# Kernel optimization log

Measured on AMD Instinct MI355X. Metric: run time of the kernel, lower is better.

Reference implementation:

```python
import jax, jax.numpy as jnp
import numpy as np

N = 50000
E = 800000
IN_C, HID_C, OUT_C = 5, 64, 32


def setup_inputs() -> dict:
    key = jax.random.key(0)
    ks = jax.random.split(key, 9)
    x = jax.random.normal(ks[0], (N, IN_C), dtype=jnp.float32)
    edge_index = jax.random.randint(ks[1], (2, E), 0, N, dtype=jnp.int64)
    # SAGEConv params: lin_l (neighbor path, has bias), lin_r (root path, no bias)
    def lin(k, fan_out, fan_in):
        s = 1.0 / np.sqrt(fan_in)
        return jax.random.uniform(k, (fan_out, fan_in), jnp.float32, -s, s)
    W1l = lin(ks[2], HID_C, IN_C); b1 = jnp.zeros((HID_C,), jnp.float32); W1r = lin(ks[3], HID_C, IN_C)
    W2l = lin(ks[4], HID_C, HID_C); b2 = jnp.zeros((HID_C,), jnp.float32); W2r = lin(ks[5], HID_C, HID_C)
    W3l = lin(ks[6], OUT_C, HID_C); b3 = jnp.zeros((OUT_C,), jnp.float32); W3r = lin(ks[7], OUT_C, HID_C)
    return {"x": x, "edge_index": edge_index,
            "W1l": W1l, "b1": b1, "W1r": W1r,
            "W2l": W2l, "b2": b2, "W2r": W2r,
            "W3l": W3l, "b3": b3, "W3r": W3r}


def _sage_conv(x, src, dst, inv_deg, Wl, bl, Wr):
    # PyG SAGEConv (aggr='mean'): out = lin_l(mean_j x_j) + lin_r(x)
    msg = x[src]                                          # [E, d_in] gather
    agg = jax.ops.segment_sum(msg, dst, num_segments=N)   # [N, d_in] scatter-add
    mean = agg * inv_deg                                  # mean aggregation
    return mean @ Wl.T + bl + x @ Wr.T


def reference(x, edge_index, W1l, b1, W1r, W2l, b2, W2r, W3l, b3, W3r):
    src, dst = edge_index[0], edge_index[1]
    deg = jax.ops.segment_sum(jnp.ones((E,), x.dtype), dst, num_segments=N)
    inv_deg = (1.0 / jnp.maximum(deg, 1.0))[:, None]      # [N, 1]
    h = jax.nn.relu(_sage_conv(x, src, dst, inv_deg, W1l, b1, W1r))
    # F.dropout(p=0.2, training=self.training): identity in eval mode
    h = jax.nn.relu(_sage_conv(h, src, dst, inv_deg, W2l, b2, W2r))
    out = _sage_conv(h, src, dst, inv_deg, W3l, b3, W3r)
    return out
```

## Files before the change

### kernel.cpp

```cpp
#include <hip/hip_runtime.h>
#include <hip/hip_fp16.h>


#define N_NODES 50000
#define N_EDGES 800000
#define IN_C 5
#define HID_C 64
#define OUT_C 32

#define NB 196
#define BCAP 6144
#define BWG 256
#define BCH (N_EDGES / BWG)

typedef __attribute__((ext_vector_type(8))) short bf16x8;
typedef __attribute__((ext_vector_type(4))) float f32x4;

__device__ __forceinline__ int rfl(int v) { return __builtin_amdgcn_readfirstlane(v); }
__device__ __forceinline__ float lanebc(float v, int l) {
    return __int_as_float(__builtin_amdgcn_readlane(__float_as_int(v), l));
}
__device__ __forceinline__ unsigned short f2bf(float f) {
    unsigned u = __float_as_uint(f);
    return (unsigned short)((u + 0x7fffu + ((u >> 16) & 1u)) >> 16);
}
__device__ __forceinline__ float bf2f(unsigned short b) {
    return __uint_as_float(((unsigned)b) << 16);
}
__device__ __forceinline__ float2 unpk_h2(unsigned u) {
    __half2 h = *(__half2*)&u;
    return __half22float2(h);
}


__global__ __launch_bounds__(256) void k_bucket(const int* __restrict__ ei,
                                                int* __restrict__ gcur,
                                                unsigned* __restrict__ ebuf) {
    __shared__ int hist[NB];
    __shared__ int loff[NB];
    __shared__ int cur[NB];
    __shared__ int gbase[NB];
    __shared__ int scanb[256];
    __shared__ unsigned stage[BCH];
    const int t = threadIdx.x;
    const int c0 = blockIdx.x * BCH;

    if (t < NB) hist[t] = 0;
    __syncthreads();
    for (int i = t; i < BCH; i += 256) {
        int d = ei[N_EDGES + c0 + i];
        atomicAdd(&hist[d >> 8], 1);
    }
    __syncthreads();
    scanb[t] = (t < NB) ? hist[t] : 0;
    __syncthreads();
#pragma unroll
    for (int o = 1; o < 256; o <<= 1) {
        int v = scanb[t];
        int a = (t >= o) ? scanb[t - o] : 0;
        __syncthreads();
        scanb[t] = v + a;
        __syncthreads();
    }
    if (t < NB) {
        int ex = (t == 0) ? 0 : scanb[t - 1];
        loff[t] = ex;
        cur[t] = ex;
        gbase[t] = atomicAdd(&gcur[t], hist[t]);
    }
    __syncthreads();
    for (int i = t; i < BCH; i += 256) {
        int d = ei[N_EDGES + c0 + i];
        int s = ei[c0 + i];
        int b = d >> 8;
        int p = atomicAdd(&cur[b], 1);
        stage[p] = ((unsigned)d << 16) | (unsigned)s;
    }
    __syncthreads();
    for (int i = t; i < BCH; i += 256) {
        unsigned ev = stage[i];
        int b = ev >> 24;
        int pos = gbase[b] + (i - loff[b]);
        if (pos < BCAP) ebuf[b * BCAP + pos] = ev;
    }
}

__global__ __launch_bounds__(256) void k_bsort(const int* __restrict__ gcur,
                                               const unsigned* __restrict__ ebuf,
                                               int* __restrict__ row_off,
                                               float* __restrict__ inv_deg,
                                               int* __restrict__ srcs) {
    __shared__ int sc[256];
    __shared__ int cnt[256];
    __shared__ int loff[256];
    __shared__ int cur[256];
    __shared__ int stage[BCAP];
    const int t = threadIdx.x;
    const int b = blockIdx.x;

    sc[t] = (t < NB) ? gcur[t] : 0;
    __syncthreads();
#pragma unroll
    for (int o = 1; o < 256; o <<= 1) {
        int v = sc[t];
        int a = (t >= o) ? sc[t - o] : 0;
        __syncthreads();
        sc[t] = v + a;
        __syncthreads();
    }
    const int base = (b == 0) ? 0 : sc[b - 1];
    const int nraw = gcur[b];
    const int n = nraw < BCAP ? nraw : BCAP;
    const int node0 = b << 8;
    const unsigned* eb = ebuf + b * BCAP;

    cnt[t] = 0;
    __syncthreads();
    for (int i = t; i < n; i += 256) atomicAdd(&cnt[(eb[i] >> 16) & 255], 1);
    __syncthreads();
    loff[t] = cnt[t];
    __syncthreads();
#pragma unroll
    for (int o = 1; o < 256; o <<= 1) {
        int v = loff[t];
        int a = (t >= o) ? loff[t - o] : 0;
        __syncthreads();
        loff[t] = v + a;
        __syncthreads();
    }
    int ex = loff[t] - cnt[t];
    cur[t] = ex;
    int node = node0 + t;
    if (node < N_NODES) {
        row_off[node] = base + ex;
        int d = cnt[t];
        inv_deg[node] = 1.0f / (float)(d > 1 ? d : 1);
    }
    if (b == 0 && t == 0) row_off[N_NODES] = N_EDGES;
    __syncthreads();
    for (int i = t; i < n; i += 256) {
        unsigned ev = eb[i];
        int p = atomicAdd(&cur[(ev >> 16) & 255], 1);
        stage[p] = (int)(ev & 0xFFFFu);
    }
    __syncthreads();
    for (int i = t; i < n; i += 256) srcs[base + i] = stage[i];
}


__global__ __launch_bounds__(256) void k_prep(
    const float* __restrict__ W2l, const float* __restrict__ W2r,
    const float* __restrict__ W3l, const float* __restrict__ W3r,
    unsigned short* __restrict__ W2hi, unsigned short* __restrict__ W2lo,
    unsigned short* __restrict__ W3hi, unsigned short* __restrict__ W3lo,
    int* __restrict__ gcur) {
    int t = blockIdx.x * 256 + threadIdx.x;
    int stride = gridDim.x * 256;
    if (blockIdx.x == 0 && threadIdx.x < NB) gcur[threadIdx.x] = 0;
    for (int p = t; p < 64 * 128; p += stride) {
        int j = p >> 7, k = p & 127;
        float w = (k < 64) ? W2l[j * 64 + k] : W2r[j * 64 + (k - 64)];
        unsigned short h = f2bf(w);
        W2hi[p] = h;
        W2lo[p] = f2bf(w - bf2f(h));
    }
    for (int p = t; p < 32 * 128; p += stride) {
        int j = p >> 7, k = p & 127;
        float w = (k < 64) ? W3l[j * 64 + k] : W3r[j * 64 + (k - 64)];
        unsigned short h = f2bf(w);
        W3hi[p] = h;
        W3lo[p] = f2bf(w - bf2f(h));
    }
}


__global__ __launch_bounds__(512) void k_layer1(
    const float* __restrict__ x, const int* __restrict__ row_off,
    const int* __restrict__ srcs, const float* __restrict__ inv_deg,
    const float* __restrict__ W1l, const float* __restrict__ b1,
    const float* __restrict__ W1r, __half* __restrict__ h1) {
    const int t = threadIdx.x;
    const int lane = t & 63;
    const int v = blockIdx.x * 8 + (t >> 6);
    if (v >= N_NODES) return;
    const int sub = lane >> 3;
    const int c = lane & 7;

    float wl[IN_C], wr[IN_C];
#pragma unroll
    for (int i = 0; i < IN_C; ++i) {
        wl[i] = W1l[lane * IN_C + i];
        wr[i] = W1r[lane * IN_C + i];
    }
    float bb = b1[lane];

    int beg = rfl(row_off[v]);
    int end = rfl(row_off[v + 1]);
    float sum = 0.f;
    for (int e = beg; e < end; e += 8) {
        int o = e + sub;
        if (o < end && c < IN_C) sum += x[srcs[o] * IN_C + c];
    }
    sum += __shfl_xor(sum, 8, 64);
    sum += __shfl_xor(sum, 16, 64);
    sum += __shfl_xor(sum, 32, 64);
    float summ = sum * inv_deg[v];
    float xv = (lane < IN_C) ? x[v * IN_C + lane] : 0.f;
    float acc = bb;
#pragma unroll
    for (int i = 0; i < IN_C; ++i) {
        acc += wl[i] * lanebc(summ, i);
        acc += wr[i] * lanebc(xv, i);
    }
    h1[v * HID_C + lane] = __float2half(fmaxf(acc, 0.f));
}


template <typename T> __device__ __forceinline__ T cvt_out(float v);
template <> __device__ __forceinline__ float cvt_out<float>(float v) { return v; }
template <> __device__ __forceinline__ __half cvt_out<__half>(float v) { return __float2half(v); }

template <int DOUT, bool RELU, typename OutT>
__global__ __launch_bounds__(256) void k_fused(
    const __half* __restrict__ h, const int* __restrict__ row_off,
    const int* __restrict__ srcs, const float* __restrict__ inv_deg,
    const unsigned short* __restrict__ Whi, const unsigned short* __restrict__ Wlo,
    const float* __restrict__ bias, OutT* __restrict__ out) {
    constexpr int AP = 136;
    __shared__ __align__(16) unsigned short Ah[16][AP];
    __shared__ __align__(16) unsigned short Al[16][AP];
    const int t = threadIdx.x;
    const int lane = t & 63;
    const int w = t >> 6;
    const int ns = lane >> 4;
    const int cg = lane & 15;
    const int node0 = blockIdx.x * 16;
    const unsigned* h32 = (const unsigned*)h;

    const int m = w * 4 + ns;
    const int v = node0 + m;
    const int beg = row_off[v];
    const int deg = row_off[v + 1] - beg;
    const unsigned* rowb = h32 + cg * 2;

    float f0 = 0.f, f1 = 0.f, f2 = 0.f, f3 = 0.f;
    for (int k = 0; k < deg; k += 4) {
        int i0 = srcs[beg + k];
        int i1 = (k + 1 < deg) ? srcs[beg + k + 1] : i0;
        int i2 = (k + 2 < deg) ? srcs[beg + k + 2] : i0;
        int i3 = (k + 3 < deg) ? srcs[beg + k + 3] : i0;
        uint2 u0 = *(const uint2*)(rowb + i0 * 32);
        uint2 u1 = *(const uint2*)(rowb + i1 * 32);
        uint2 u2 = *(const uint2*)(rowb + i2 * 32);
        uint2 u3 = *(const uint2*)(rowb + i3 * 32);
        float2 a0 = unpk_h2(u0.x), b0 = unpk_h2(u0.y);
        f0 += a0.x; f1 += a0.y; f2 += b0.x; f3 += b0.y;
        if (k + 1 < deg) {
            float2 a = unpk_h2(u1.x), b = unpk_h2(u1.y);
            f0 += a.x; f1 += a.y; f2 += b.x; f3 += b.y;
        }
        if (k + 2 < deg) {
            float2 a = unpk_h2(u2.x), b = unpk_h2(u2.y);
            f0 += a.x; f1 += a.y; f2 += b.x; f3 += b.y;
        }
        if (k + 3 < deg) {
            float2 a = unpk_h2(u3.x), b = unpk_h2(u3.y);
            f0 += a.x; f1 += a.y; f2 += b.x; f3 += b.y;
        }
    }

    uint2 ur = *(const uint2*)(rowb + v * 32);
    float2 r0 = unpk_h2(ur.x), r1 = unpk_h2(ur.y);
    float idg = inv_deg[v];
    float m0 = f0 * idg, m1 = f1 * idg, m2 = f2 * idg, m3 = f3 * idg;

    {
        unsigned short a0 = f2bf(m0), a1 = f2bf(m1), a2 = f2bf(m2), a3 = f2bf(m3);
        uint2 hi, lo;
        hi.x = (unsigned)a0 | ((unsigned)a1 << 16);
        hi.y = (unsigned)a2 | ((unsigned)a3 << 16);
        lo.x = (unsigned)f2bf(m0 - bf2f(a0)) | ((unsigned)f2bf(m1 - bf2f(a1)) << 16);
        lo.y = (unsigned)f2bf(m2 - bf2f(a2)) | ((unsigned)f2bf(m3 - bf2f(a3)) << 16);
        *(uint2*)&Ah[m][cg * 4] = hi;
        *(uint2*)&Al[m][cg * 4] = lo;
    }
    {
        unsigned short a0 = f2bf(r0.x), a1 = f2bf(r0.y), a2 = f2bf(r1.x), a3 = f2bf(r1.y);
        uint2 hi, lo;
        hi.x = (unsigned)a0 | ((unsigned)a1 << 16);
        hi.y = (unsigned)a2 | ((unsigned)a3 << 16);
        lo.x = (unsigned)f2bf(r0.x - bf2f(a0)) | ((unsigned)f2bf(r0.y - bf2f(a1)) << 16);
        lo.y = (unsigned)f2bf(r1.x - bf2f(a2)) | ((unsigned)f2bf(r1.y - bf2f(a3)) << 16);
        *(uint2*)&Ah[m][64 + cg * 4] = hi;
        *(uint2*)&Al[m][64 + cg * 4] = lo;
    }
    __syncthreads();

    constexpr int NT = DOUT / 16;
    if (w < NT) {
        const int r = lane & 15;
        const int quad = lane >> 4;
        f32x4 acc = (f32x4){0.f, 0.f, 0.f, 0.f};
#pragma unroll
        for (int ks = 0; ks < 4; ++ks) {
            bf16x8 ah = *(const bf16x8*)&Ah[r][ks * 32 + quad * 8];
            bf16x8 al = *(const bf16x8*)&Al[r][ks * 32 + quad * 8];
            const size_t wb = ((size_t)(w * 16 + r)) * 128 + ks * 32 + quad * 8;
            bf16x8 bh = *(const bf16x8*)(Whi + wb);
            bf16x8 bl = *(const bf16x8*)(Wlo + wb);
            acc = __builtin_amdgcn_mfma_f32_16x16x32_bf16(ah, bh, acc, 0, 0, 0);
            acc = __builtin_amdgcn_mfma_f32_16x16x32_bf16(ah, bl, acc, 0, 0, 0);
            acc = __builtin_amdgcn_mfma_f32_16x16x32_bf16(al, bh, acc, 0, 0, 0);
        }
        float bv = bias[w * 16 + r];
#pragma unroll
        for (int g = 0; g < 4; ++g) {
            int mm = quad * 4 + g;
            float vv = acc[g] + bv;
            if (RELU) vv = fmaxf(vv, 0.f);
            out[(size_t)(node0 + mm) * DOUT + w * 16 + r] = cvt_out<OutT>(vv);
        }
    }
}


extern "C" void kernel_launch(void* const* d_in, const int* in_sizes, int n_in,
                              void* d_out, int out_size, void* d_ws, size_t ws_size,
                              hipStream_t stream) {
    const float* x   = (const float*)d_in[0];
    const int*   ei  = (const int*)d_in[1];
    const float* W1l = (const float*)d_in[2];
    const float* b1  = (const float*)d_in[3];
    const float* W1r = (const float*)d_in[4];
    const float* W2l = (const float*)d_in[5];
    const float* b2  = (const float*)d_in[6];
    const float* W2r = (const float*)d_in[7];
    const float* W3l = (const float*)d_in[8];
    const float* b3  = (const float*)d_in[9];
    const float* W3r = (const float*)d_in[10];

    char* ws = (char*)d_ws;
    size_t off = 0;
    auto alloc = [&](size_t bytes) -> char* {
        char* p = ws + off;
        off += (bytes + 255) & ~(size_t)255;
        return p;
    };
    int*      gcur   = (int*)alloc(NB * sizeof(int));
    int*      rowoff = (int*)alloc((N_NODES + 1) * sizeof(int));
    float*    invdeg = (float*)alloc(N_NODES * sizeof(float));
    int*      srcs   = (int*)alloc(N_EDGES * sizeof(int));
    unsigned* ebuf   = (unsigned*)alloc((size_t)NB * BCAP * sizeof(unsigned));
    __half*   h1     = (__half*)alloc((size_t)N_NODES * HID_C * sizeof(__half));
    __half*   h2     = (__half*)alloc((size_t)N_NODES * HID_C * sizeof(__half));
    unsigned short* W2hi = (unsigned short*)alloc(64 * 128 * 2);
    unsigned short* W2lo = (unsigned short*)alloc(64 * 128 * 2);
    unsigned short* W3hi = (unsigned short*)alloc(32 * 128 * 2);
    unsigned short* W3lo = (unsigned short*)alloc(32 * 128 * 2);

    k_prep<<<dim3(48), dim3(256), 0, stream>>>(W2l, W2r, W3l, W3r,
                                               W2hi, W2lo, W3hi, W3lo, gcur);
    k_bucket<<<dim3(BWG), dim3(256), 0, stream>>>(ei, gcur, ebuf);
    k_bsort<<<dim3(NB), dim3(256), 0, stream>>>(gcur, ebuf, rowoff, invdeg, srcs);

    k_layer1<<<dim3((N_NODES + 7) / 8), dim3(512), 0, stream>>>(
        x, rowoff, srcs, invdeg, W1l, b1, W1r, h1);

    k_fused<HID_C, true, __half><<<dim3(N_NODES / 16), dim3(256), 0, stream>>>(
        h1, rowoff, srcs, invdeg, W2hi, W2lo, b2, h2);

    k_fused<OUT_C, false, float><<<dim3(N_NODES / 16), dim3(256), 0, stream>>>(
        h2, rowoff, srcs, invdeg, W3hi, W3lo, b3, (float*)d_out);
}
```

Measured before the change: 185.9 us.

## Fuse all stages into one cooperative persistent kernel with grid syncs

Replaces the six separate kernel launches with a single cooperative persistent kernel that runs weight prep, bucketing, bucket sort, layer 1 and the two fused SAGE layers, separated by grid-wide syncs. Each phase becomes a grid-stride loop over its original work units, and shared memory is a union of the per-phase layouts. The aim is to remove launch overhead and inter-kernel gaps. In exchange, the grid is limited to resident occupancy, the large shared-memory union may cut blocks per CU for the gather phases, and each grid sync has its own cost. A non-cooperative fallback path keeps the original multi-kernel sequence.

```diff
diff --git a/kernel.cpp b/kernel.cpp
--- a/kernel.cpp
+++ b/kernel.cpp
@@ -1,5 +1,8 @@
 #include <hip/hip_runtime.h>
 #include <hip/hip_fp16.h>
+#include <hip/hip_cooperative_groups.h>
+
+namespace cgx = cooperative_groups;
 
 
 #define N_NODES 50000
@@ -13,6 +16,8 @@
 #define BWG 256
 #define BCH (N_EDGES / BWG)
 
+#define NTHR 256
+
 typedef __attribute__((ext_vector_type(8))) short bf16x8;
 typedef __attribute__((ext_vector_type(4))) float f32x4;
 
@@ -32,131 +37,31 @@
     return __half22float2(h);
 }
 
-
-__global__ __launch_bounds__(256) void k_bucket(const int* __restrict__ ei,
-                                                int* __restrict__ gcur,
-                                                unsigned* __restrict__ ebuf) {
-    __shared__ int hist[NB];
-    __shared__ int loff[NB];
-    __shared__ int cur[NB];
-    __shared__ int gbase[NB];
-    __shared__ int scanb[256];
-    __shared__ unsigned stage[BCH];
-    const int t = threadIdx.x;
-    const int c0 = blockIdx.x * BCH;
-
-    if (t < NB) hist[t] = 0;
-    __syncthreads();
-    for (int i = t; i < BCH; i += 256) {
-        int d = ei[N_EDGES + c0 + i];
-        atomicAdd(&hist[d >> 8], 1);
-    }
-    __syncthreads();
-    scanb[t] = (t < NB) ? hist[t] : 0;
-    __syncthreads();
-#pragma unroll
-    for (int o = 1; o < 256; o <<= 1) {
-        int v = scanb[t];
-        int a = (t >= o) ? scanb[t - o] : 0;
-        __syncthreads();
-        scanb[t] = v + a;
-        __syncthreads();
-    }
-    if (t < NB) {
-        int ex = (t == 0) ? 0 : scanb[t - 1];
-        loff[t] = ex;
-        cur[t] = ex;
-        gbase[t] = atomicAdd(&gcur[t], hist[t]);
-    }
-    __syncthreads();
-    for (int i = t; i < BCH; i += 256) {
-        int d = ei[N_EDGES + c0 + i];
-        int s = ei[c0 + i];
-        int b = d >> 8;
-        int p = atomicAdd(&cur[b], 1);
-        stage[p] = ((unsigned)d << 16) | (unsigned)s;
-    }
-    __syncthreads();
-    for (int i = t; i < BCH; i += 256) {
-        unsigned ev = stage[i];
-        int b = ev >> 24;
-        int pos = gbase[b] + (i - loff[b]);
-        if (pos < BCAP) ebuf[b * BCAP + pos] = ev;
-    }
-}
-
-__global__ __launch_bounds__(256) void k_bsort(const int* __restrict__ gcur,
-                                               const unsigned* __restrict__ ebuf,
-                                               int* __restrict__ row_off,
-                                               float* __restrict__ inv_deg,
-                                               int* __restrict__ srcs) {
-    __shared__ int sc[256];
-    __shared__ int cnt[256];
-    __shared__ int loff[256];
-    __shared__ int cur[256];
-    __shared__ int stage[BCAP];
-    const int t = threadIdx.x;
-    const int b = blockIdx.x;
-
-    sc[t] = (t < NB) ? gcur[t] : 0;
-    __syncthreads();
-#pragma unroll
-    for (int o = 1; o < 256; o <<= 1) {
-        int v = sc[t];
-        int a = (t >= o) ? sc[t - o] : 0;
-        __syncthreads();
-        sc[t] = v + a;
-        __syncthreads();
-    }
-    const int base = (b == 0) ? 0 : sc[b - 1];
-    const int nraw = gcur[b];
-    const int n = nraw < BCAP ? nraw : BCAP;
-    const int node0 = b << 8;
-    const unsigned* eb = ebuf + b * BCAP;
-
-    cnt[t] = 0;
-    __syncthreads();
-    for (int i = t; i < n; i += 256) atomicAdd(&cnt[(eb[i] >> 16) & 255], 1);
-    __syncthreads();
-    loff[t] = cnt[t];
-    __syncthreads();
-#pragma unroll
-    for (int o = 1; o < 256; o <<= 1) {
-        int v = loff[t];
-        int a = (t >= o) ? loff[t - o] : 0;
-        __syncthreads();
-        loff[t] = v + a;
-        __syncthreads();
-    }
-    int ex = loff[t] - cnt[t];
-    cur[t] = ex;
-    int node = node0 + t;
-    if (node < N_NODES) {
-        row_off[node] = base + ex;
-        int d = cnt[t];
-        inv_deg[node] = 1.0f / (float)(d > 1 ? d : 1);
-    }
-    if (b == 0 && t == 0) row_off[N_NODES] = N_EDGES;
-    __syncthreads();
-    for (int i = t; i < n; i += 256) {
-        unsigned ev = eb[i];
-        int p = atomicAdd(&cur[(ev >> 16) & 255], 1);
-        stage[p] = (int)(ev & 0xFFFFu);
-    }
-    __syncthreads();
-    for (int i = t; i < n; i += 256) srcs[base + i] = stage[i];
-}
-
-
-__global__ __launch_bounds__(256) void k_prep(
-    const float* __restrict__ W2l, const float* __restrict__ W2r,
-    const float* __restrict__ W3l, const float* __restrict__ W3r,
-    unsigned short* __restrict__ W2hi, unsigned short* __restrict__ W2lo,
-    unsigned short* __restrict__ W3hi, unsigned short* __restrict__ W3lo,
-    int* __restrict__ gcur) {
-    int t = blockIdx.x * 256 + threadIdx.x;
-    int stride = gridDim.x * 256;
-    if (blockIdx.x == 0 && threadIdx.x < NB) gcur[threadIdx.x] = 0;
+struct SmBucket {
+    int hist[NB], loff[NB], cur[NB], gbase[NB];
+    int scanb[256];
+    unsigned stage[BCH];
+};
+struct SmSort {
+    int sc[256], cnt[256], loff[256], cur[256];
+    int stage[BCAP];
+};
+struct SmFused {
+    unsigned short Ah[16][136], Al[16][136];
+};
+union SMem {
+    SmBucket b;
+    SmSort s;
+    SmFused f;
+};
+
+
+__device__ void prep_phase(const float* __restrict__ W2l, const float* __restrict__ W2r,
+                           const float* __restrict__ W3l, const float* __restrict__ W3r,
+                           unsigned short* __restrict__ W2hi, unsigned short* __restrict__ W2lo,
+                           unsigned short* __restrict__ W3hi, unsigned short* __restrict__ W3lo) {
+    const int t = blockIdx.x * NTHR + threadIdx.x;
+    const int stride = gridDim.x * NTHR;
     for (int p = t; p < 64 * 128; p += stride) {
         int j = p >> 7, k = p & 127;
         float w = (k < 64) ? W2l[j * 64 + k] : W2r[j * 64 + (k - 64)];
@@ -173,16 +78,113 @@
     }
 }
 
-
-__global__ __launch_bounds__(512) void k_layer1(
-    const float* __restrict__ x, const int* __restrict__ row_off,
-    const int* __restrict__ srcs, const float* __restrict__ inv_deg,
-    const float* __restrict__ W1l, const float* __restrict__ b1,
-    const float* __restrict__ W1r, __half* __restrict__ h1) {
+__device__ void bucket_chunk(SmBucket& sm, int chunk, const int* __restrict__ ei,
+                             int* __restrict__ gcur, unsigned* __restrict__ ebuf) {
+    const int t = threadIdx.x;
+    const int c0 = chunk * BCH;
+    if (t < NB) sm.hist[t] = 0;
+    __syncthreads();
+    for (int i = t; i < BCH; i += 256) {
+        int d = ei[N_EDGES + c0 + i];
+        atomicAdd(&sm.hist[d >> 8], 1);
+    }
+    __syncthreads();
+    sm.scanb[t] = (t < NB) ? sm.hist[t] : 0;
+    __syncthreads();
+#pragma unroll
+    for (int o = 1; o < 256; o <<= 1) {
+        int v = sm.scanb[t];
+        int a = (t >= o) ? sm.scanb[t - o] : 0;
+        __syncthreads();
+        sm.scanb[t] = v + a;
+        __syncthreads();
+    }
+    if (t < NB) {
+        int ex = (t == 0) ? 0 : sm.scanb[t - 1];
+        sm.loff[t] = ex;
+        sm.cur[t] = ex;
+        sm.gbase[t] = atomicAdd(&gcur[t], sm.hist[t]);
+    }
+    __syncthreads();
+    for (int i = t; i < BCH; i += 256) {
+        int d = ei[N_EDGES + c0 + i];
+        int s = ei[c0 + i];
+        int b = d >> 8;
+        int p = atomicAdd(&sm.cur[b], 1);
+        sm.stage[p] = ((unsigned)d << 16) | (unsigned)s;
+    }
+    __syncthreads();
+    for (int i = t; i < BCH; i += 256) {
+        unsigned ev = sm.stage[i];
+        int b = ev >> 24;
+        int pos = sm.gbase[b] + (i - sm.loff[b]);
+        if (pos < BCAP) ebuf[b * BCAP + pos] = ev;
+    }
+    __syncthreads();
+}
+
+__device__ void bsort_bucket(SmSort& sm, int b, const int* __restrict__ gcur,
+                             const unsigned* __restrict__ ebuf, int* __restrict__ row_off,
+                             float* __restrict__ inv_deg, int* __restrict__ srcs) {
+    const int t = threadIdx.x;
+    sm.sc[t] = (t < NB) ? gcur[t] : 0;
+    __syncthreads();
+#pragma unroll
+    for (int o = 1; o < 256; o <<= 1) {
+        int v = sm.sc[t];
+        int a = (t >= o) ? sm.sc[t - o] : 0;
+        __syncthreads();
+        sm.sc[t] = v + a;
+        __syncthreads();
+    }
+    const int base = (b == 0) ? 0 : sm.sc[b - 1];
+    const int nraw = gcur[b];
+    const int n = nraw < BCAP ? nraw : BCAP;
+    const int node0 = b << 8;
+    const unsigned* eb = ebuf + b * BCAP;
+
+    sm.cnt[t] = 0;
+    __syncthreads();
+    for (int i = t; i < n; i += 256) atomicAdd(&sm.cnt[(eb[i] >> 16) & 255], 1);
+    __syncthreads();
+    sm.loff[t] = sm.cnt[t];
+    __syncthreads();
+#pragma unroll
+    for (int o = 1; o < 256; o <<= 1) {
+        int v = sm.loff[t];
+        int a = (t >= o) ? sm.loff[t - o] : 0;
+        __syncthreads();
+        sm.loff[t] = v + a;
+        __syncthreads();
+    }
+    int ex = sm.loff[t] - sm.cnt[t];
+    sm.cur[t] = ex;
+    int node = node0 + t;
+    if (node < N_NODES) {
+        row_off[node] = base + ex;
+        int d = sm.cnt[t];
+        inv_deg[node] = 1.0f / (float)(d > 1 ? d : 1);
+    }
+    if (b == 0 && t == 0) row_off[N_NODES] = N_EDGES;
+    __syncthreads();
+    for (int i = t; i < n; i += 256) {
+        unsigned ev = eb[i];
+        int p = atomicAdd(&sm.cur[(ev >> 16) & 255], 1);
+        sm.stage[p] = (int)(ev & 0xFFFFu);
+    }
+    __syncthreads();
+    for (int i = t; i < n; i += 256) srcs[base + i] = sm.stage[i];
+    __syncthreads();
+}
+
+__device__ void layer1_phase(const float* __restrict__ x, const int* __restrict__ row_off,
+                             const int* __restrict__ srcs, const float* __restrict__ inv_deg,
+                             const float* __restrict__ W1l, const float* __restrict__ b1,
+                             const float* __restrict__ W1r, __half* __restrict__ h1) {
     const int t = threadIdx.x;
     const int lane = t & 63;
-    const int v = blockIdx.x * 8 + (t >> 6);
-    if (v >= N_NODES) return;
+    const int wid = blockIdx.x * 4 + (t >> 6);
+    const int nw = gridDim.x * 4;
     const int sub = lane >> 3;
     const int c = lane & 7;
 
@@ -194,133 +196,201 @@
     }
     float bb = b1[lane];
 
-    int beg = rfl(row_off[v]);
-    int end = rfl(row_off[v + 1]);
-    float sum = 0.f;
-    for (int e = beg; e < end; e += 8) {
-        int o = e + sub;
-        if (o < end && c < IN_C) sum += x[srcs[o] * IN_C + c];
-    }
-    sum += __shfl_xor(sum, 8, 64);
-    sum += __shfl_xor(sum, 16, 64);
-    sum += __shfl_xor(sum, 32, 64);
-    float summ = sum * inv_deg[v];
-    float xv = (lane < IN_C) ? x[v * IN_C + lane] : 0.f;
-    float acc = bb;
-#pragma unroll
-    for (int i = 0; i < IN_C; ++i) {
-        acc += wl[i] * lanebc(summ, i);
-        acc += wr[i] * lanebc(xv, i);
-    }
-    h1[v * HID_C + lane] = __float2half(fmaxf(acc, 0.f));
-}
-
+    for (int v = wid; v < N_NODES; v += nw) {
+        int beg = rfl(row_off[v]);
+        int end = rfl(row_off[v + 1]);
+        float sum = 0.f;
+        for (int e = beg; e < end; e += 8) {
+            int o = e + sub;
+            if (o < end && c < IN_C) sum += x[srcs[o] * IN_C + c];
+        }
+        sum += __shfl_xor(sum, 8, 64);
+        sum += __shfl_xor(sum, 16, 64);
+        sum += __shfl_xor(sum, 32, 64);
+        float summ = sum * inv_deg[v];
+        float xv = (lane < IN_C) ? x[v * IN_C + lane] : 0.f;
+        float acc = bb;
+#pragma unroll
+        for (int i = 0; i < IN_C; ++i) {
+            acc += wl[i] * lanebc(summ, i);
+            acc += wr[i] * lanebc(xv, i);
+        }
+        h1[v * HID_C + lane] = __float2half(fmaxf(acc, 0.f));
+    }
+}
 
 template <typename T> __device__ __forceinline__ T cvt_out(float v);
 template <> __device__ __forceinline__ float cvt_out<float>(float v) { return v; }
 template <> __device__ __forceinline__ __half cvt_out<__half>(float v) { return __float2half(v); }
 
 template <int DOUT, bool RELU, typename OutT>
-__global__ __launch_bounds__(256) void k_fused(
-    const __half* __restrict__ h, const int* __restrict__ row_off,
-    const int* __restrict__ srcs, const float* __restrict__ inv_deg,
-    const unsigned short* __restrict__ Whi, const unsigned short* __restrict__ Wlo,
-    const float* __restrict__ bias, OutT* __restrict__ out) {
-    constexpr int AP = 136;
-    __shared__ __align__(16) unsigned short Ah[16][AP];
-    __shared__ __align__(16) unsigned short Al[16][AP];
+__device__ void fused_phase(SmFused& sm, const __half* __restrict__ h,
+                            const int* __restrict__ row_off, const int* __restrict__ srcs,
+                            const float* __restrict__ inv_deg,
+                            const unsigned short* __restrict__ Whi,
+                            const unsigned short* __restrict__ Wlo,
+                            const float* __restrict__ bias, OutT* __restrict__ out) {
     const int t = threadIdx.x;
     const int lane = t & 63;
     const int w = t >> 6;
     const int ns = lane >> 4;
-    const int cg = lane & 15;
-    const int node0 = blockIdx.x * 16;
+    const int cgi = lane & 15;
     const unsigned* h32 = (const unsigned*)h;
-
-    const int m = w * 4 + ns;
-    const int v = node0 + m;
-    const int beg = row_off[v];
-    const int deg = row_off[v + 1] - beg;
-    const unsigned* rowb = h32 + cg * 2;
-
-    float f0 = 0.f, f1 = 0.f, f2 = 0.f, f3 = 0.f;
-    for (int k = 0; k < deg; k += 4) {
-        int i0 = srcs[beg + k];
-        int i1 = (k + 1 < deg) ? srcs[beg + k + 1] : i0;
-        int i2 = (k + 2 < deg) ? srcs[beg + k + 2] : i0;
-        int i3 = (k + 3 < deg) ? srcs[beg + k + 3] : i0;
-        uint2 u0 = *(const uint2*)(rowb + i0 * 32);
-        uint2 u1 = *(const uint2*)(rowb + i1 * 32);
-        uint2 u2 = *(const uint2*)(rowb + i2 * 32);
-        uint2 u3 = *(const uint2*)(rowb + i3 * 32);
-        float2 a0 = unpk_h2(u0.x), b0 = unpk_h2(u0.y);
-        f0 += a0.x; f1 += a0.y; f2 += b0.x; f3 += b0.y;
-        if (k + 1 < deg) {
-            float2 a = unpk_h2(u1.x), b = unpk_h2(u1.y);
-            f0 += a.x; f1 += a.y; f2 += b.x; f3 += b.y;
-        }
-        if (k + 2 < deg) {
-            float2 a = unpk_h2(u2.x), b = unpk_h2(u2.y);
-            f0 += a.x; f1 += a.y; f2 += b.x; f3 += b.y;
-        }
-        if (k + 3 < deg) {
-            float2 a = unpk_h2(u3.x), b = unpk_h2(u3.y);
-            f0 += a.x; f1 += a.y; f2 += b.x; f3 += b.y;
-        }
-    }
-
-    uint2 ur = *(const uint2*)(rowb + v * 32);
-    float2 r0 = unpk_h2(ur.x), r1 = unpk_h2(ur.y);
-    float idg = inv_deg[v];
-    float m0 = f0 * idg, m1 = f1 * idg, m2 = f2 * idg, m3 = f3 * idg;
-
-    {
-        unsigned short a0 = f2bf(m0), a1 = f2bf(m1), a2 = f2bf(m2), a3 = f2bf(m3);
-        uint2 hi, lo;
-        hi.x = (unsigned)a0 | ((unsigned)a1 << 16);
-        hi.y = (unsigned)a2 | ((unsigned)a3 << 16);
-        lo.x = (unsigned)f2bf(m0 - bf2f(a0)) | ((unsigned)f2bf(m1 - bf2f(a1)) << 16);
-        lo.y = (unsigned)f2bf(m2 - bf2f(a2)) | ((unsigned)f2bf(m3 - bf2f(a3)) << 16);
-        *(uint2*)&Ah[m][cg * 4] = hi;
-        *(uint2*)&Al[m][cg * 4] = lo;
-    }
-    {
-        unsigned short a0 = f2bf(r0.x), a1 = f2bf(r0.y), a2 = f2bf(r1.x), a3 = f2bf(r1.y);
-        uint2 hi, lo;
-        hi.x = (unsigned)a0 | ((unsigned)a1 << 16);
-        hi.y = (unsigned)a2 | ((unsigned)a3 << 16);
-        lo.x = (unsigned)f2bf(r0.x - bf2f(a0)) | ((unsigned)f2bf(r0.y - bf2f(a1)) << 16);
-        lo.y = (unsigned)f2bf(r1.x - bf2f(a2)) | ((unsigned)f2bf(r1.y - bf2f(a3)) << 16);
-        *(uint2*)&Ah[m][64 + cg * 4] = hi;
-        *(uint2*)&Al[m][64 + cg * 4] = lo;
-    }
-    __syncthreads();
-
-    constexpr int NT = DOUT / 16;
-    if (w < NT) {
-        const int r = lane & 15;
-        const int quad = lane >> 4;
-        f32x4 acc = (f32x4){0.f, 0.f, 0.f, 0.f};
-#pragma unroll
-        for (int ks = 0; ks < 4; ++ks) {
-            bf16x8 ah = *(const bf16x8*)&Ah[r][ks * 32 + quad * 8];
-            bf16x8 al = *(const bf16x8*)&Al[r][ks * 32 + quad * 8];
-            const size_t wb = ((size_t)(w * 16 + r)) * 128 + ks * 32 + quad * 8;
-            bf16x8 bh = *(const bf16x8*)(Whi + wb);
-            bf16x8 bl = *(const bf16x8*)(Wlo + wb);
-            acc = __builtin_amdgcn_mfma_f32_16x16x32_bf16(ah, bh, acc, 0, 0, 0);
-            acc = __builtin_amdgcn_mfma_f32_16x16x32_bf16(ah, bl, acc, 0, 0, 0);
-            acc = __builtin_amdgcn_mfma_f32_16x16x32_bf16(al, bh, acc, 0, 0, 0);
-        }
-        float bv = bias[w * 16 + r];
-#pragma unroll
-        for (int g = 0; g < 4; ++g) {
-            int mm = quad * 4 + g;
-            float vv = acc[g] + bv;
-            if (RELU) vv = fmaxf(vv, 0.f);
-            out[(size_t)(node0 + mm) * DOUT + w * 16 + r] = cvt_out<OutT>(vv);
-        }
-    }
+    const unsigned* rowb = h32 + cgi * 2;
+
+    for (int tile = blockIdx.x; tile < N_NODES / 16; tile += gridDim.x) {
+        const int node0 = tile * 16;
+        const int m = w * 4 + ns;
+        const int v = node0 + m;
+        const int beg = row_off[v];
+        const int deg = row_off[v + 1] - beg;
+
+        float f0 = 0.f, f1 = 0.f, f2 = 0.f, f3 = 0.f;
+        for (int k = 0; k < deg; k += 4) {
+            int i0 = srcs[beg + k];
+            int i1 = (k + 1 < deg) ? srcs[beg + k + 1] : i0;
+            int i2 = (k + 2 < deg) ? srcs[beg + k + 2] : i0;
+            int i3 = (k + 3 < deg) ? srcs[beg + k + 3] : i0;
+            uint2 u0 = *(const uint2*)(rowb + i0 * 32);
+            uint2 u1 = *(const uint2*)(rowb + i1 * 32);
+            uint2 u2 = *(const uint2*)(rowb + i2 * 32);
+            uint2 u3 = *(const uint2*)(rowb + i3 * 32);
+            float2 a0 = unpk_h2(u0.x), b0 = unpk_h2(u0.y);
+            f0 += a0.x; f1 += a0.y; f2 += b0.x; f3 += b0.y;
+            if (k + 1 < deg) {
+                float2 a = unpk_h2(u1.x), b = unpk_h2(u1.y);
+                f0 += a.x; f1 += a.y; f2 += b.x; f3 += b.y;
+            }
+            if (k + 2 < deg) {
+                float2 a = unpk_h2(u2.x), b = unpk_h2(u2.y);
+                f0 += a.x; f1 += a.y; f2 += b.x; f3 += b.y;
+            }
+            if (k + 3 < deg) {
+                float2 a = unpk_h2(u3.x), b = unpk_h2(u3.y);
+                f0 += a.x; f1 += a.y; f2 += b.x; f3 += b.y;
+            }
+        }
+
+        uint2 ur = *(const uint2*)(rowb + v * 32);
+        float2 r0 = unpk_h2(ur.x), r1 = unpk_h2(ur.y);
+        float idg = inv_deg[v];
+        float m0 = f0 * idg, m1 = f1 * idg, m2 = f2 * idg, m3 = f3 * idg;
+
+        {
+            unsigned short a0 = f2bf(m0), a1 = f2bf(m1), a2 = f2bf(m2), a3 = f2bf(m3);
+            uint2 hi, lo;
+            hi.x = (unsigned)a0 | ((unsigned)a1 << 16);
+            hi.y = (unsigned)a2 | ((unsigned)a3 << 16);
+            lo.x = (unsigned)f2bf(m0 - bf2f(a0)) | ((unsigned)f2bf(m1 - bf2f(a1)) << 16);
+            lo.y = (unsigned)f2bf(m2 - bf2f(a2)) | ((unsigned)f2bf(m3 - bf2f(a3)) << 16);
+            *(uint2*)&sm.Ah[m][cgi * 4] = hi;
+            *(uint2*)&sm.Al[m][cgi * 4] = lo;
+        }
+        {
+            unsigned short a0 = f2bf(r0.x), a1 = f2bf(r0.y), a2 = f2bf(r1.x), a3 = f2bf(r1.y);
+            uint2 hi, lo;
+            hi.x = (unsigned)a0 | ((unsigned)a1 << 16);
+            hi.y = (unsigned)a2 | ((unsigned)a3 << 16);
+            lo.x = (unsigned)f2bf(r0.x - bf2f(a0)) | ((unsigned)f2bf(r0.y - bf2f(a1)) << 16);
+            lo.y = (unsigned)f2bf(r1.x - bf2f(a2)) | ((unsigned)f2bf(r1.y - bf2f(a3)) << 16);
+            *(uint2*)&sm.Ah[m][64 + cgi * 4] = hi;
+            *(uint2*)&sm.Al[m][64 + cgi * 4] = lo;
+        }
+        __syncthreads();
+
+        constexpr int NT = DOUT / 16;
+        if (w < NT) {
+            const int r = lane & 15;
+            const int quad = lane >> 4;
+            f32x4 acc = (f32x4){0.f, 0.f, 0.f, 0.f};
+#pragma unroll
+            for (int ks = 0; ks < 4; ++ks) {
+                bf16x8 ah = *(const bf16x8*)&sm.Ah[r][ks * 32 + quad * 8];
+                bf16x8 al = *(const bf16x8*)&sm.Al[r][ks * 32 + quad * 8];
+                const size_t wb = ((size_t)(w * 16 + r)) * 128 + ks * 32 + quad * 8;
+                bf16x8 bh = *(const bf16x8*)(Whi + wb);
+                bf16x8 bl = *(const bf16x8*)(Wlo + wb);
+                acc = __builtin_amdgcn_mfma_f32_16x16x32_bf16(ah, bh, acc, 0, 0, 0);
+                acc = __builtin_amdgcn_mfma_f32_16x16x32_bf16(ah, bl, acc, 0, 0, 0);
+                acc = __builtin_amdgcn_mfma_f32_16x16x32_bf16(al, bh, acc, 0, 0, 0);
+            }
+            float bv = bias[w * 16 + r];
+#pragma unroll
+            for (int g = 0; g < 4; ++g) {
+                int mm = quad * 4 + g;
+                float vv = acc[g] + bv;
+                if (RELU) vv = fmaxf(vv, 0.f);
+                out[(size_t)(node0 + mm) * DOUT + w * 16 + r] = cvt_out<OutT>(vv);
+            }
+        }
+        __syncthreads();
+    }
+}
+
+
+__global__ __launch_bounds__(NTHR, 4) void k_mega(
+    const float* x, const int* ei,
+    const float* W1l, const float* b1, const float* W1r,
+    const float* W2l, const float* b2, const float* W2r,
+    const float* W3l, const float* b3, const float* W3r,
+    int* gcur, int* rowoff, float* invdeg, int* srcs, unsigned* ebuf,
+    __half* h1, __half* h2,
+    unsigned short* W2hi, unsigned short* W2lo,
+    unsigned short* W3hi, unsigned short* W3lo,
+    float* out) {
+    __shared__ __align__(16) SMem sm;
+    cgx::grid_group grid = cgx::this_grid();
+
+    prep_phase(W2l, W2r, W3l, W3r, W2hi, W2lo, W3hi, W3lo);
+    for (int c = blockIdx.x; c < BWG; c += gridDim.x)
+        bucket_chunk(sm.b, c, ei, gcur, ebuf);
+    grid.sync();
+
+    for (int b = blockIdx.x; b < NB; b += gridDim.x)
+        bsort_bucket(sm.s, b, gcur, ebuf, rowoff, invdeg, srcs);
+    grid.sync();
+
+    layer1_phase(x, rowoff, srcs, invdeg, W1l, b1, W1r, h1);
+    grid.sync();
+
+    fused_phase<HID_C, true, __half>(sm.f, h1, rowoff, srcs, invdeg, W2hi, W2lo, b2, h2);
+    grid.sync();
+
+    fused_phase<OUT_C, false, float>(sm.f, h2, rowoff, srcs, invdeg, W3hi, W3lo, b3, out);
+}
+
+
+__global__ __launch_bounds__(NTHR) void g_prep(
+    const float* W2l, const float* W2r, const float* W3l, const float* W3r,
+    unsigned short* W2hi, unsigned short* W2lo,
+    unsigned short* W3hi, unsigned short* W3lo) {
+    prep_phase(W2l, W2r, W3l, W3r, W2hi, W2lo, W3hi, W3lo);
+}
+
+__global__ __launch_bounds__(NTHR) void g_bucket(const int* ei, int* gcur, unsigned* ebuf) {
+    __shared__ __align__(16) SmBucket sm;
+    bucket_chunk(sm, blockIdx.x, ei, gcur, ebuf);
+}
+
+__global__ __launch_bounds__(NTHR) void g_bsort(const int* gcur, const unsigned* ebuf,
+                                                int* rowoff, float* invdeg, int* srcs) {
+    __shared__ __align__(16) SmSort sm;
+    bsort_bucket(sm, blockIdx.x, gcur, ebuf, rowoff, invdeg, srcs);
+}
+
+__global__ __launch_bounds__(NTHR) void g_layer1(
+    const float* x, const int* rowoff, const int* srcs, const float* invdeg,
+    const float* W1l, const float* b1, const float* W1r, __half* h1) {
+    layer1_phase(x, rowoff, srcs, invdeg, W1l, b1, W1r, h1);
+}
+
+template <int DOUT, bool RELU, typename OutT>
+__global__ __launch_bounds__(NTHR) void g_fused(
+    const __half* h, const int* rowoff, const int* srcs, const float* invdeg,
+    const unsigned short* Whi, const unsigned short* Wlo,
+    const float* bias, OutT* out) {
+    __shared__ __align__(16) SmFused sm;
+    fused_phase<DOUT, RELU, OutT>(sm, h, rowoff, srcs, invdeg, Whi, Wlo, bias, out);
 }
 
 
@@ -357,18 +427,43 @@
     unsigned short* W2lo = (unsigned short*)alloc(64 * 128 * 2);
     unsigned short* W3hi = (unsigned short*)alloc(32 * 128 * 2);
     unsigned short* W3lo = (unsigned short*)alloc(32 * 128 * 2);
-
-    k_prep<<<dim3(48), dim3(256), 0, stream>>>(W2l, W2r, W3l, W3r,
-                                               W2hi, W2lo, W3hi, W3lo, gcur);
-    k_bucket<<<dim3(BWG), dim3(256), 0, stream>>>(ei, gcur, ebuf);
-    k_bsort<<<dim3(NB), dim3(256), 0, stream>>>(gcur, ebuf, rowoff, invdeg, srcs);
-
-    k_layer1<<<dim3((N_NODES + 7) / 8), dim3(512), 0, stream>>>(
+    float* outp = (float*)d_out;
+
+    hipMemsetAsync(gcur, 0, NB * sizeof(int), stream);
+
+    int dev = 0;
+    (void)hipGetDevice(&dev);
+    int coop = 0, ncu = 0, bpc = 0;
+    (void)hipDeviceGetAttribute(&coop, hipDeviceAttributeCooperativeLaunch, dev);
+    (void)hipDeviceGetAttribute(&ncu, hipDeviceAttributeMultiprocessorCount, dev);
+    hipError_t oe = hipOccupancyMaxActiveBlocksPerMultiprocessor(&bpc, k_mega, NTHR, 0);
+
+    if (coop && oe == hipSuccess && bpc >= 1 && ncu >= 1) {
+        int nblk = bpc * ncu;
+        if (nblk > 1024) nblk = 1024;
+        void* args[] = {
+            (void*)&x, (void*)&ei,
+            (void*)&W1l, (void*)&b1, (void*)&W1r,
+            (void*)&W2l, (void*)&b2, (void*)&W2r,
+            (void*)&W3l, (void*)&b3, (void*)&W3r,
+            (void*)&gcur, (void*)&rowoff, (void*)&invdeg, (void*)&srcs, (void*)&ebuf,
+            (void*)&h1, (void*)&h2,
+            (void*)&W2hi, (void*)&W2lo, (void*)&W3hi, (void*)&W3lo,
+            (void*)&outp,
+        };
+        hipError_t le = hipLaunchCooperativeKernel((const void*)k_mega, dim3(nblk),
+                                                   dim3(NTHR), args, 0, stream);
+        if (le == hipSuccess) return;
+    }
+
+    g_prep<<<dim3(48), dim3(NTHR), 0, stream>>>(W2l, W2r, W3l, W3r,
+                                                W2hi, W2lo, W3hi, W3lo);
+    g_bucket<<<dim3(BWG), dim3(NTHR), 0, stream>>>(ei, gcur, ebuf);
+    g_bsort<<<dim3(NB), dim3(NTHR), 0, stream>>>(gcur, ebuf, rowoff, invdeg, srcs);
+    g_layer1<<<dim3(N_NODES / 4), dim3(NTHR), 0, stream>>>(
         x, rowoff, srcs, invdeg, W1l, b1, W1r, h1);
-
-    k_fused<HID_C, true, __half><<<dim3(N_NODES / 16), dim3(256), 0, stream>>>(
+    g_fused<HID_C, true, __half><<<dim3(N_NODES / 16), dim3(NTHR), 0, stream>>>(
         h1, rowoff, srcs, invdeg, W2hi, W2lo, b2, h2);
-
-    k_fused<OUT_C, false, float><<<dim3(N_NODES / 16), dim3(256), 0, stream>>>(
-        h2, rowoff, srcs, invdeg, W3hi, W3lo, b3, (float*)d_out);
-}
+    g_fused<OUT_C, false, float><<<dim3(N_NODES / 16), dim3(NTHR), 0, stream>>>(
+        h2, rowoff, srcs, invdeg, W3hi, W3lo, b3, outp);
+}
```

New measurement: 581.0 us. +212.6%, slower.

## Widen gather to 16-byte loads and process 32 nodes per fused block

Applied to the files above, without the earlier changes.

The fused SAGE kernels now give each node 8 lanes that each load a uint4 (8 halves) per neighbor, in place of 16 lanes loading 8 bytes. A block therefore covers 32 nodes, and the MFMA stage loops over two row halves so that every wave gets tiles, including the OUT_C layer. Layer 1 moves to 256-thread blocks, and k_prep is moved earlier in the file. The wider loads should cut gather instruction count and make better use of idle waves in the matmul. The cost is fewer threads in flight per edge, bounds checks for the partial last block, and a larger LDS footprint.

```diff
diff --git a/kernel.cpp b/kernel.cpp
--- a/kernel.cpp
+++ b/kernel.cpp
@@ -30,6 +30,32 @@
 __device__ __forceinline__ float2 unpk_h2(unsigned u) {
     __half2 h = *(__half2*)&u;
     return __half22float2(h);
+}
+
+
+__global__ __launch_bounds__(256) void k_prep(
+    const float* __restrict__ W2l, const float* __restrict__ W2r,
+    const float* __restrict__ W3l, const float* __restrict__ W3r,
+    unsigned short* __restrict__ W2hi, unsigned short* __restrict__ W2lo,
+    unsigned short* __restrict__ W3hi, unsigned short* __restrict__ W3lo,
+    int* __restrict__ gcur) {
+    if (blockIdx.x == 0 && threadIdx.x < NB) gcur[threadIdx.x] = 0;
+    const int t = blockIdx.x * 256 + threadIdx.x;
+    const int stride = gridDim.x * 256;
+    for (int p = t; p < 64 * 128; p += stride) {
+        int j = p >> 7, k = p & 127;
+        float w = (k < 64) ? W2l[j * 64 + k] : W2r[j * 64 + (k - 64)];
+        unsigned short h = f2bf(w);
+        W2hi[p] = h;
+        W2lo[p] = f2bf(w - bf2f(h));
+    }
+    for (int p = t; p < 32 * 128; p += stride) {
+        int j = p >> 7, k = p & 127;
+        float w = (k < 64) ? W3l[j * 64 + k] : W3r[j * 64 + (k - 64)];
+        unsigned short h = f2bf(w);
+        W3hi[p] = h;
+        W3lo[p] = f2bf(w - bf2f(h));
+    }
 }
 
 
@@ -148,40 +174,14 @@
 }
 
 
-__global__ __launch_bounds__(256) void k_prep(
-    const float* __restrict__ W2l, const float* __restrict__ W2r,
-    const float* __restrict__ W3l, const float* __restrict__ W3r,
-    unsigned short* __restrict__ W2hi, unsigned short* __restrict__ W2lo,
-    unsigned short* __restrict__ W3hi, unsigned short* __restrict__ W3lo,
-    int* __restrict__ gcur) {
-    int t = blockIdx.x * 256 + threadIdx.x;
-    int stride = gridDim.x * 256;
-    if (blockIdx.x == 0 && threadIdx.x < NB) gcur[threadIdx.x] = 0;
-    for (int p = t; p < 64 * 128; p += stride) {
-        int j = p >> 7, k = p & 127;
-        float w = (k < 64) ? W2l[j * 64 + k] : W2r[j * 64 + (k - 64)];
-        unsigned short h = f2bf(w);
-        W2hi[p] = h;
-        W2lo[p] = f2bf(w - bf2f(h));
-    }
-    for (int p = t; p < 32 * 128; p += stride) {
-        int j = p >> 7, k = p & 127;
-        float w = (k < 64) ? W3l[j * 64 + k] : W3r[j * 64 + (k - 64)];
-        unsigned short h = f2bf(w);
-        W3hi[p] = h;
-        W3lo[p] = f2bf(w - bf2f(h));
-    }
-}
-
-
-__global__ __launch_bounds__(512) void k_layer1(
+__global__ __launch_bounds__(256) void k_layer1(
     const float* __restrict__ x, const int* __restrict__ row_off,
     const int* __restrict__ srcs, const float* __restrict__ inv_deg,
     const float* __restrict__ W1l, const float* __restrict__ b1,
     const float* __restrict__ W1r, __half* __restrict__ h1) {
     const int t = threadIdx.x;
     const int lane = t & 63;
-    const int v = blockIdx.x * 8 + (t >> 6);
+    const int v = blockIdx.x * 4 + (t >> 6);
     if (v >= N_NODES) return;
     const int sub = lane >> 3;
     const int c = lane & 7;
@@ -226,99 +226,135 @@
     const int* __restrict__ srcs, const float* __restrict__ inv_deg,
     const unsigned short* __restrict__ Whi, const unsigned short* __restrict__ Wlo,
     const float* __restrict__ bias, OutT* __restrict__ out) {
-    constexpr int AP = 136;
-    __shared__ __align__(16) unsigned short Ah[16][AP];
-    __shared__ __align__(16) unsigned short Al[16][AP];
+    constexpr int AP = 152;
+    __shared__ __align__(16) unsigned short Ah[32][AP];
+    __shared__ __align__(16) unsigned short Al[32][AP];
     const int t = threadIdx.x;
     const int lane = t & 63;
     const int w = t >> 6;
-    const int ns = lane >> 4;
-    const int cg = lane & 15;
-    const int node0 = blockIdx.x * 16;
-    const unsigned* h32 = (const unsigned*)h;
-
-    const int m = w * 4 + ns;
+    const int ns = lane >> 3;
+    const int cg = lane & 7;
+    const int node0 = blockIdx.x * 32;
+    const int m = w * 8 + ns;
     const int v = node0 + m;
-    const int beg = row_off[v];
-    const int deg = row_off[v + 1] - beg;
-    const unsigned* rowb = h32 + cg * 2;
-
-    float f0 = 0.f, f1 = 0.f, f2 = 0.f, f3 = 0.f;
+    const bool valid = v < N_NODES;
+    const uint4* h4 = (const uint4*)h;
+
+    int beg = 0, deg = 0;
+    if (valid) {
+        beg = row_off[v];
+        deg = row_off[v + 1] - beg;
+    }
+
+    float s0 = 0.f, s1 = 0.f, s2 = 0.f, s3 = 0.f;
+    float s4 = 0.f, s5 = 0.f, s6 = 0.f, s7 = 0.f;
     for (int k = 0; k < deg; k += 4) {
         int i0 = srcs[beg + k];
         int i1 = (k + 1 < deg) ? srcs[beg + k + 1] : i0;
         int i2 = (k + 2 < deg) ? srcs[beg + k + 2] : i0;
         int i3 = (k + 3 < deg) ? srcs[beg + k + 3] : i0;
-        uint2 u0 = *(const uint2*)(rowb + i0 * 32);
-        uint2 u1 = *(const uint2*)(rowb + i1 * 32);
-        uint2 u2 = *(const uint2*)(rowb + i2 * 32);
-        uint2 u3 = *(const uint2*)(rowb + i3 * 32);
-        float2 a0 = unpk_h2(u0.x), b0 = unpk_h2(u0.y);
-        f0 += a0.x; f1 += a0.y; f2 += b0.x; f3 += b0.y;
+        uint4 u0 = h4[i0 * 8 + cg];
+        uint4 u1 = h4[i1 * 8 + cg];
+        uint4 u2 = h4[i2 * 8 + cg];
+        uint4 u3 = h4[i3 * 8 + cg];
+        {
+            float2 a = unpk_h2(u0.x), b = unpk_h2(u0.y);
+            float2 c = unpk_h2(u0.z), d = unpk_h2(u0.w);
+            s0 += a.x; s1 += a.y; s2 += b.x; s3 += b.y;
+            s4 += c.x; s5 += c.y; s6 += d.x; s7 += d.y;
+        }
         if (k + 1 < deg) {
             float2 a = unpk_h2(u1.x), b = unpk_h2(u1.y);
-            f0 += a.x; f1 += a.y; f2 += b.x; f3 += b.y;
+            float2 c = unpk_h2(u1.z), d = unpk_h2(u1.w);
+            s0 += a.x; s1 += a.y; s2 += b.x; s3 += b.y;
+            s4 += c.x; s5 += c.y; s6 += d.x; s7 += d.y;
         }
         if (k + 2 < deg) {
             float2 a = unpk_h2(u2.x), b = unpk_h2(u2.y);
-            f0 += a.x; f1 += a.y; f2 += b.x; f3 += b.y;
+            float2 c = unpk_h2(u2.z), d = unpk_h2(u2.w);
+            s0 += a.x; s1 += a.y; s2 += b.x; s3 += b.y;
+            s4 += c.x; s5 += c.y; s6 += d.x; s7 += d.y;
         }
         if (k + 3 < deg) {
             float2 a = unpk_h2(u3.x), b = unpk_h2(u3.y);
-            f0 += a.x; f1 += a.y; f2 += b.x; f3 += b.y;
-        }
-    }
-
-    uint2 ur = *(const uint2*)(rowb + v * 32);
-    float2 r0 = unpk_h2(ur.x), r1 = unpk_h2(ur.y);
-    float idg = inv_deg[v];
-    float m0 = f0 * idg, m1 = f1 * idg, m2 = f2 * idg, m3 = f3 * idg;
+            float2 c = unpk_h2(u3.z), d = unpk_h2(u3.w);
+            s0 += a.x; s1 += a.y; s2 += b.x; s3 += b.y;
+            s4 += c.x; s5 += c.y; s6 += d.x; s7 += d.y;
+        }
+    }
+
+    uint4 ur = make_uint4(0u, 0u, 0u, 0u);
+    float idg = 0.f;
+    if (valid) {
+        ur = h4[v * 8 + cg];
+        idg = inv_deg[v];
+    }
+    float m0 = s0 * idg, m1 = s1 * idg, m2 = s2 * idg, m3 = s3 * idg;
+    float m4 = s4 * idg, m5 = s5 * idg, m6 = s6 * idg, m7 = s7 * idg;
 
     {
         unsigned short a0 = f2bf(m0), a1 = f2bf(m1), a2 = f2bf(m2), a3 = f2bf(m3);
-        uint2 hi, lo;
+        unsigned short a4 = f2bf(m4), a5 = f2bf(m5), a6 = f2bf(m6), a7 = f2bf(m7);
+        uint4 hi, lo;
         hi.x = (unsigned)a0 | ((unsigned)a1 << 16);
         hi.y = (unsigned)a2 | ((unsigned)a3 << 16);
+        hi.z = (unsigned)a4 | ((unsigned)a5 << 16);
+        hi.w = (unsigned)a6 | ((unsigned)a7 << 16);
         lo.x = (unsigned)f2bf(m0 - bf2f(a0)) | ((unsigned)f2bf(m1 - bf2f(a1)) << 16);
         lo.y = (unsigned)f2bf(m2 - bf2f(a2)) | ((unsigned)f2bf(m3 - bf2f(a3)) << 16);
-        *(uint2*)&Ah[m][cg * 4] = hi;
-        *(uint2*)&Al[m][cg * 4] = lo;
+        lo.z = (unsigned)f2bf(m4 - bf2f(a4)) | ((unsigned)f2bf(m5 - bf2f(a5)) << 16);
+        lo.w = (unsigned)f2bf(m6 - bf2f(a6)) | ((unsigned)f2bf(m7 - bf2f(a7)) << 16);
+        *(uint4*)&Ah[m][cg * 8] = hi;
+        *(uint4*)&Al[m][cg * 8] = lo;
     }
     {
-        unsigned short a0 = f2bf(r0.x), a1 = f2bf(r0.y), a2 = f2bf(r1.x), a3 = f2bf(r1.y);
-        uint2 hi, lo;
+        float2 p0 = unpk_h2(ur.x), p1 = unpk_h2(ur.y);
+        float2 p2 = unpk_h2(ur.z), p3 = unpk_h2(ur.w);
+        unsigned short a0 = f2bf(p0.x), a1 = f2bf(p0.y), a2 = f2bf(p1.x), a3 = f2bf(p1.y);
+        unsigned short a4 = f2bf(p2.x), a5 = f2bf(p2.y), a6 = f2bf(p3.x), a7 = f2bf(p3.y);
+        uint4 hi, lo;
         hi.x = (unsigned)a0 | ((unsigned)a1 << 16);
         hi.y = (unsigned)a2 | ((unsigned)a3 << 16);
-        lo.x = (unsigned)f2bf(r0.x - bf2f(a0)) | ((unsigned)f2bf(r0.y - bf2f(a1)) << 16);
-        lo.y = (unsigned)f2bf(r1.x - bf2f(a2)) | ((unsigned)f2bf(r1.y - bf2f(a3)) << 16);
-        *(uint2*)&Ah[m][64 + cg * 4] = hi;
-        *(uint2*)&Al[m][64 + cg * 4] = lo;
-    }
-    __syncthreads();
-
-    constexpr int NT = DOUT / 16;
-    if (w < NT) {
-        const int r = lane & 15;
-        const int quad = lane >> 4;
+        hi.z = (unsigned)a4 | ((unsigned)a5 << 16);
+        hi.w = (unsigned)a6 | ((unsigned)a7 << 16);
+        lo.x = (unsigned)f2bf(p0.x - bf2f(a0)) | ((unsigned)f2bf(p0.y - bf2f(a1)) << 16);
+        lo.y = (unsigned)f2bf(p1.x - bf2f(a2)) | ((unsigned)f2bf(p1.y - bf2f(a3)) << 16);
+        lo.z = (unsigned)f2bf(p2.x - bf2f(a4)) | ((unsigned)f2bf(p2.y - bf2f(a5)) << 16);
+        lo.w = (unsigned)f2bf(p3.x - bf2f(a6)) | ((unsigned)f2bf(p3.y - bf2f(a7)) << 16);
+        *(uint4*)&Ah[m][64 + cg * 8] = hi;
+        *(uint4*)&Al[m][64 + cg * 8] = lo;
+    }
+    __syncthreads();
+
+    constexpr int CT = DOUT / 16;
+    constexpr int NTILES = 2 * CT;
+    const int r = lane & 15;
+    const int quad = lane >> 4;
+#pragma unroll
+    for (int ti = w; ti < NTILES; ti += 4) {
+        const int n = ti % CT;
+        const int rh = ti / CT;
         f32x4 acc = (f32x4){0.f, 0.f, 0.f, 0.f};
 #pragma unroll
         for (int ks = 0; ks < 4; ++ks) {
-            bf16x8 ah = *(const bf16x8*)&Ah[r][ks * 32 + quad * 8];
-            bf16x8 al = *(const bf16x8*)&Al[r][ks * 32 + quad * 8];
-            const size_t wb = ((size_t)(w * 16 + r)) * 128 + ks * 32 + quad * 8;
+            bf16x8 ah = *(const bf16x8*)&Ah[rh * 16 + r][ks * 32 + quad * 8];
+            bf16x8 al = *(const bf16x8*)&Al[rh * 16 + r][ks * 32 + quad * 8];
+            const size_t wb = ((size_t)(n * 16 + r)) * 128 + ks * 32 + quad * 8;
             bf16x8 bh = *(const bf16x8*)(Whi + wb);
             bf16x8 bl = *(const bf16x8*)(Wlo + wb);
             acc = __builtin_amdgcn_mfma_f32_16x16x32_bf16(ah, bh, acc, 0, 0, 0);
             acc = __builtin_amdgcn_mfma_f32_16x16x32_bf16(ah, bl, acc, 0, 0, 0);
             acc = __builtin_amdgcn_mfma_f32_16x16x32_bf16(al, bh, acc, 0, 0, 0);
         }
-        float bv = bias[w * 16 + r];
+        float bv = bias[n * 16 + r];
 #pragma unroll
         for (int g = 0; g < 4; ++g) {
-            int mm = quad * 4 + g;
-            float vv = acc[g] + bv;
-            if (RELU) vv = fmaxf(vv, 0.f);
-            out[(size_t)(node0 + mm) * DOUT + w * 16 + r] = cvt_out<OutT>(vv);
+            int node = node0 + rh * 16 + quad * 4 + g;
+            if (node < N_NODES) {
+                float vv = acc[g] + bv;
+                if (RELU) vv = fmaxf(vv, 0.f);
+                out[(size_t)node * DOUT + n * 16 + r] = cvt_out<OutT>(vv);
+            }
         }
     }
 }
@@ -363,12 +399,13 @@
     k_bucket<<<dim3(BWG), dim3(256), 0, stream>>>(ei, gcur, ebuf);
     k_bsort<<<dim3(NB), dim3(256), 0, stream>>>(gcur, ebuf, rowoff, invdeg, srcs);
 
-    k_layer1<<<dim3((N_NODES + 7) / 8), dim3(512), 0, stream>>>(
+    k_layer1<<<dim3(N_NODES / 4), dim3(256), 0, stream>>>(
         x, rowoff, srcs, invdeg, W1l, b1, W1r, h1);
 
-    k_fused<HID_C, true, __half><<<dim3(N_NODES / 16), dim3(256), 0, stream>>>(
+    const int FT = (N_NODES + 31) / 32;
+    k_fused<HID_C, true, __half><<<dim3(FT), dim3(256), 0, stream>>>(
         h1, rowoff, srcs, invdeg, W2hi, W2lo, b2, h2);
 
-    k_fused<OUT_C, false, float><<<dim3(N_NODES / 16), dim3(256), 0, stream>>>(
+    k_fused<OUT_C, false, float><<<dim3(FT), dim3(256), 0, stream>>>(
         h2, rowoff, srcs, invdeg, W3hi, W3lo, b3, (float*)d_out);
 }
```

Result: faster. 172.9 us (-7.0%).
